# Kernel tuning notes

Measured on AMD Instinct MI355X. Metric: run time of the kernel, lower is better.

Reference implementation:

```python
import jax, jax.numpy as jnp
import numpy as np

HK, HV, D, K = 16, 32, 128, 4  # key heads, value heads, head dim, conv kernel
EPS = 1e-6


def setup_inputs() -> dict:
    key = jax.random.key(0)
    ks = jax.random.split(key, 8)
    B = 128
    C = D * (2 * HK + HV)  # qkv_size = 8192
    return {
        "mixed_qkv": jax.random.normal(ks[0], (B, C), jnp.float32),
        "a": jax.random.normal(ks[1], (B, HV), jnp.float32),
        "b": jax.random.normal(ks[2], (B, HV), jnp.float32),
        "conv_state": jax.random.normal(ks[3], (B, K - 1, C), jnp.float32),
        "ssm_state": jax.random.normal(ks[4], (B, HV, D, D), jnp.float32) * 0.1,
        "conv_weights": jax.random.normal(ks[5], (C, K), jnp.float32) * 0.1,
        "dt_bias": jax.random.normal(ks[6], (HV,), jnp.float32),
        "A_log": jax.random.normal(ks[7], (HV,), jnp.float32),
    }


def _l2norm(x):
    return x * jax.lax.rsqrt(jnp.sum(x * x, axis=-1, keepdims=True) + EPS)


def reference(mixed_qkv, a, b, conv_state, ssm_state, conv_weights, dt_bias, A_log):
    B = mixed_qkv.shape[0]
    # --- causal_conv1d_update (single decode token) ---
    # window: last K-1 cached tokens + current token, per channel
    window = jnp.concatenate([conv_state, mixed_qkv[:, None, :]], axis=1)  # [B, K, C]
    xconv = jax.nn.silu(jnp.einsum("bkc,ck->bc", window, conv_weights))  # [B, C]

    # --- split q/k/v heads ---
    qkv = xconv.reshape(B, 2 * HK + HV, D)
    q, k, v = qkv[:, :HK], qkv[:, HK:2 * HK], qkv[:, 2 * HK:]  # [B,HK,D]x2, [B,HV,D]

    # --- fused_gdn_gating ---
    g = -jnp.exp(A_log) * jax.nn.softplus(a + dt_bias)  # [B, HV]
    beta = jax.nn.sigmoid(b)                            # [B, HV]

    # --- fused_recurrent_gated_delta_rule, one step, qk l2norm + scale ---
    scale = D ** -0.5
    q = _l2norm(q) * scale
    k = _l2norm(k)
    rep = HV // HK  # GQA replication of q/k heads
    q = jnp.repeat(q, rep, axis=1)  # [B, HV, D]
    k = jnp.repeat(k, rep, axis=1)  # [B, HV, D]

    S = ssm_state * jnp.exp(g)[:, :, None, None]        # decay: [B,HV,Dv,Dk]
    kv_mem = jnp.einsum("bhvk,bhk->bhv", S, k)          # state readout along k
    delta = (v - kv_mem) * beta[:, :, None]             # delta rule correction
    S = S + delta[:, :, :, None] * k[:, :, None, :]     # rank-1 state update
    out = jnp.einsum("bhvk,bhk->bhv", S, q)             # [B, HV, Dv]
    return out
```

## Files before the change

kernel.cpp:

```cpp
#include <hip/hip_runtime.h>
#include <math.h>

#define HK 16
#define HV 32
#define DD 128
#define CC 8192
#define EPSN 1e-6f
#define QSCALE 0.08838834764831845f

__global__ __launch_bounds__(256) void prep_kernel(
    const float* __restrict__ mixed_qkv,
    const float* __restrict__ a_in,
    const float* __restrict__ b_in,
    const float* __restrict__ conv_state,
    const float* __restrict__ conv_weights,
    const float* __restrict__ dt_bias,
    const float* __restrict__ A_log,
    float* __restrict__ ws_q, float* __restrict__ ws_k, float* __restrict__ ws_v,
    float* __restrict__ ws_g, float* __restrict__ ws_beta)
{
    const int b   = blockIdx.x;
    const int tid = threadIdx.x;
    __shared__ float xconv[CC];

    const float* cs = conv_state + (size_t)b * 3 * CC;
    const float* mq = mixed_qkv  + (size_t)b * CC;

    for (int idx = tid; idx < CC; idx += 256) {
        float4 w = *reinterpret_cast<const float4*>(conv_weights + (size_t)idx * 4);
        float x = cs[idx] * w.x + cs[CC + idx] * w.y + cs[2 * CC + idx] * w.z
                + mq[idx] * w.w;
        xconv[idx] = x / (1.0f + expf(-x));
    }

    if (tid < HV) {
        float av = a_in[b * HV + tid] + dt_bias[tid];
        float sp = (av > 20.0f) ? av : log1pf(expf(av));
        ws_g[b * HV + tid]    = -expf(A_log[tid]) * sp;
        ws_beta[b * HV + tid] = 1.0f / (1.0f + expf(-b_in[b * HV + tid]));
    }
    __syncthreads();

    const int h   = tid >> 3;
    const int sub = tid & 7;
    const float* base = xconv + h * DD;
    float ssq = 0.f;
    #pragma unroll
    for (int i = 0; i < 16; ++i) {
        float xv = base[sub + 8 * i];
        ssq += xv * xv;
    }
    ssq += __shfl_xor(ssq, 1);
    ssq += __shfl_xor(ssq, 2);
    ssq += __shfl_xor(ssq, 4);
    float r = rsqrtf(ssq + EPSN);
    float factor = (h < HK) ? r * QSCALE : r;
    float* dst = (h < HK) ? (ws_q + ((size_t)b * HK + h) * DD)
                          : (ws_k + ((size_t)b * HK + (h - HK)) * DD);
    #pragma unroll
    for (int i = 0; i < 16; ++i)
        dst[sub + 8 * i] = base[sub + 8 * i] * factor;

    float* vdst = ws_v + (size_t)b * HV * DD;
    for (int idx = tid; idx < HV * DD; idx += 256)
        vdst[idx] = xconv[2 * HK * DD + idx];
}

__global__ __launch_bounds__(256) void update_kernel(
    const float* __restrict__ ssm_state,
    const float* __restrict__ ws_q, const float* __restrict__ ws_k,
    const float* __restrict__ ws_v, const float* __restrict__ ws_g,
    const float* __restrict__ ws_beta,
    float* __restrict__ out)
{
    const int bh  = blockIdx.x;
    const int b   = bh >> 5;
    const int h   = bh & 31;
    const int qh  = h >> 1;
    const int tid = threadIdx.x;
    const int col = (tid & 31) * 4;
    const int rb  = tid >> 5;

    __shared__ float dk[DD], dq[DD];

    const float4 kf = *reinterpret_cast<const float4*>(ws_k + ((size_t)b * HK + qh) * DD + col);
    const float4 qf = *reinterpret_cast<const float4*>(ws_q + ((size_t)b * HK + qh) * DD + col);

    float kq = kf.x * qf.x + kf.y * qf.y + kf.z * qf.z + kf.w * qf.w;
    kq += __shfl_xor(kq, 16);
    kq += __shfl_xor(kq, 8);
    kq += __shfl_xor(kq, 4);
    kq += __shfl_xor(kq, 2);
    kq += __shfl_xor(kq, 1);

    const float* S = ssm_state + (size_t)bh * DD * DD;
    #pragma unroll
    for (int c = 0; c < 16; ++c) {
        const int row = c * 8 + rb;
        float4 s = *reinterpret_cast<const float4*>(S + (size_t)row * DD + col);
        float pk = s.x * kf.x + s.y * kf.y + s.z * kf.z + s.w * kf.w;
        float pq = s.x * qf.x + s.y * qf.y + s.z * qf.z + s.w * qf.w;
        #pragma unroll
        for (int m = 16; m >= 1; m >>= 1) {
            pk += __shfl_xor(pk, m);
            pq += __shfl_xor(pq, m);
        }
        if ((tid & 31) == 0) { dk[row] = pk; dq[row] = pq; }
    }
    __syncthreads();

    if (tid < DD) {
        float eg   = expf(ws_g[bh]);
        float beta = ws_beta[bh];
        float vv   = ws_v[(size_t)bh * DD + tid];
        float delta = (vv - eg * dk[tid]) * beta;
        out[(size_t)bh * DD + tid] = eg * dq[tid] + delta * kq;
    }
}

extern "C" void kernel_launch(void* const* d_in, const int* in_sizes, int n_in,
                              void* d_out, int out_size, void* d_ws, size_t ws_size,
                              hipStream_t stream) {
    const float* mixed_qkv    = (const float*)d_in[0];
    const float* a_in         = (const float*)d_in[1];
    const float* b_in         = (const float*)d_in[2];
    const float* conv_state   = (const float*)d_in[3];
    const float* ssm_state    = (const float*)d_in[4];
    const float* conv_weights = (const float*)d_in[5];
    const float* dt_bias      = (const float*)d_in[6];
    const float* A_log        = (const float*)d_in[7];
    float* out = (float*)d_out;

    const int B = in_sizes[1] / HV;

    float* ws_q    = (float*)d_ws;
    float* ws_k    = ws_q + (size_t)B * HK * DD;
    float* ws_v    = ws_k + (size_t)B * HK * DD;
    float* ws_g    = ws_v + (size_t)B * HV * DD;
    float* ws_beta = ws_g + (size_t)B * HV;

    prep_kernel<<<B, 256, 0, stream>>>(mixed_qkv, a_in, b_in, conv_state,
                                       conv_weights, dt_bias, A_log,
                                       ws_q, ws_k, ws_v, ws_g, ws_beta);
    update_kernel<<<B * HV, 256, 0, stream>>>(ssm_state, ws_q, ws_k, ws_v,
                                              ws_g, ws_beta, out);
}
```

Before: 59.50 us.

## Fuse conv prep and state update into one kernel with a single matvec

```diff
diff --git a/kernel.cpp b/kernel.cpp
--- a/kernel.cpp
+++ b/kernel.cpp
@@ -1,121 +1,110 @@
 #include <hip/hip_runtime.h>
 #include <math.h>
 
-#define HK 16
-#define HV 32
-#define DD 128
-#define CC 8192
+#define HKn 16
+#define HVn 32
+#define DDn 128
+#define CCn 8192
 #define EPSN 1e-6f
 #define QSCALE 0.08838834764831845f
 
-__global__ __launch_bounds__(256) void prep_kernel(
+__global__ __launch_bounds__(256) void fused_gdn_decode(
     const float* __restrict__ mixed_qkv,
     const float* __restrict__ a_in,
     const float* __restrict__ b_in,
     const float* __restrict__ conv_state,
+    const float* __restrict__ ssm_state,
     const float* __restrict__ conv_weights,
     const float* __restrict__ dt_bias,
     const float* __restrict__ A_log,
-    float* __restrict__ ws_q, float* __restrict__ ws_k, float* __restrict__ ws_v,
-    float* __restrict__ ws_g, float* __restrict__ ws_beta)
+    float* __restrict__ out)
 {
-    const int b   = blockIdx.x;
-    const int tid = threadIdx.x;
-    __shared__ float xconv[CC];
+    const int bh = blockIdx.x;
+    const int b  = bh >> 5;
+    const int h  = bh & 31;
+    const int qh = h >> 1;
+    const int t  = threadIdx.x;
 
-    const float* cs = conv_state + (size_t)b * 3 * CC;
-    const float* mq = mixed_qkv  + (size_t)b * CC;
+    __shared__ float wv[DDn];
+    __shared__ float vb[DDn];
+    __shared__ float po[DDn];
+    __shared__ float red[6];
 
-    for (int idx = tid; idx < CC; idx += 256) {
-        float4 w = *reinterpret_cast<const float4*>(conv_weights + (size_t)idx * 4);
-        float x = cs[idx] * w.x + cs[CC + idx] * w.y + cs[2 * CC + idx] * w.z
-                + mq[idx] * w.w;
-        xconv[idx] = x / (1.0f + expf(-x));
-    }
+    const float* cs = conv_state + (size_t)b * 3 * CCn;
+    const float* mq = mixed_qkv  + (size_t)b * CCn;
 
-    if (tid < HV) {
-        float av = a_in[b * HV + tid] + dt_bias[tid];
-        float sp = (av > 20.0f) ? av : log1pf(expf(av));
-        ws_g[b * HV + tid]    = -expf(A_log[tid]) * sp;
-        ws_beta[b * HV + tid] = 1.0f / (1.0f + expf(-b_in[b * HV + tid]));
+    float xq = 0.f, xk = 0.f, bkq = 0.f;
+
+    if (t < DDn) {
+        const int cq = qh * DDn + t;
+        const int ck = (HKn + qh) * DDn + t;
+        float4 w = *reinterpret_cast<const float4*>(conv_weights + (size_t)cq * 4);
+        float x = cs[cq] * w.x + cs[CCn + cq] * w.y + cs[2 * CCn + cq] * w.z + mq[cq] * w.w;
+        xq = x / (1.f + expf(-x));
+        w = *reinterpret_cast<const float4*>(conv_weights + (size_t)ck * 4);
+        x = cs[ck] * w.x + cs[CCn + ck] * w.y + cs[2 * CCn + ck] * w.z + mq[ck] * w.w;
+        xk = x / (1.f + expf(-x));
+
+        float sqq = xq * xq, skk = xk * xk, sqk = xq * xk;
+        #pragma unroll
+        for (int m = 1; m <= 32; m <<= 1) {
+            sqq += __shfl_xor(sqq, m);
+            skk += __shfl_xor(skk, m);
+            sqk += __shfl_xor(sqk, m);
+        }
+        if ((t & 63) == 0) {
+            const int wv_ = t >> 6;
+            red[wv_ * 3 + 0] = sqq;
+            red[wv_ * 3 + 1] = skk;
+            red[wv_ * 3 + 2] = sqk;
+        }
+    } else {
+        const int cv = (2 * HKn + h) * DDn + (t - DDn);
+        float4 w = *reinterpret_cast<const float4*>(conv_weights + (size_t)cv * 4);
+        float x = cs[cv] * w.x + cs[CCn + cv] * w.y + cs[2 * CCn + cv] * w.z + mq[cv] * w.w;
+        vb[t - DDn] = x / (1.f + expf(-x));
     }
     __syncthreads();
 
-    const int h   = tid >> 3;
-    const int sub = tid & 7;
-    const float* base = xconv + h * DD;
-    float ssq = 0.f;
-    #pragma unroll
-    for (int i = 0; i < 16; ++i) {
-        float xv = base[sub + 8 * i];
-        ssq += xv * xv;
-    }
-    ssq += __shfl_xor(ssq, 1);
-    ssq += __shfl_xor(ssq, 2);
-    ssq += __shfl_xor(ssq, 4);
-    float r = rsqrtf(ssq + EPSN);
-    float factor = (h < HK) ? r * QSCALE : r;
-    float* dst = (h < HK) ? (ws_q + ((size_t)b * HK + h) * DD)
-                          : (ws_k + ((size_t)b * HK + (h - HK)) * DD);
-    #pragma unroll
-    for (int i = 0; i < 16; ++i)
-        dst[sub + 8 * i] = base[sub + 8 * i] * factor;
-
-    float* vdst = ws_v + (size_t)b * HV * DD;
-    for (int idx = tid; idx < HV * DD; idx += 256)
-        vdst[idx] = xconv[2 * HK * DD + idx];
-}
-
-__global__ __launch_bounds__(256) void update_kernel(
-    const float* __restrict__ ssm_state,
-    const float* __restrict__ ws_q, const float* __restrict__ ws_k,
-    const float* __restrict__ ws_v, const float* __restrict__ ws_g,
-    const float* __restrict__ ws_beta,
-    float* __restrict__ out)
-{
-    const int bh  = blockIdx.x;
-    const int b   = bh >> 5;
-    const int h   = bh & 31;
-    const int qh  = h >> 1;
-    const int tid = threadIdx.x;
-    const int col = (tid & 31) * 4;
-    const int rb  = tid >> 5;
-
-    __shared__ float dk[DD], dq[DD];
-
-    const float4 kf = *reinterpret_cast<const float4*>(ws_k + ((size_t)b * HK + qh) * DD + col);
-    const float4 qf = *reinterpret_cast<const float4*>(ws_q + ((size_t)b * HK + qh) * DD + col);
-
-    float kq = kf.x * qf.x + kf.y * qf.y + kf.z * qf.z + kf.w * qf.w;
-    kq += __shfl_xor(kq, 16);
-    kq += __shfl_xor(kq, 8);
-    kq += __shfl_xor(kq, 4);
-    kq += __shfl_xor(kq, 2);
-    kq += __shfl_xor(kq, 1);
-
-    const float* S = ssm_state + (size_t)bh * DD * DD;
-    #pragma unroll
-    for (int c = 0; c < 16; ++c) {
-        const int row = c * 8 + rb;
-        float4 s = *reinterpret_cast<const float4*>(S + (size_t)row * DD + col);
-        float pk = s.x * kf.x + s.y * kf.y + s.z * kf.z + s.w * kf.w;
-        float pq = s.x * qf.x + s.y * qf.y + s.z * qf.z + s.w * qf.w;
-        #pragma unroll
-        for (int m = 16; m >= 1; m >>= 1) {
-            pk += __shfl_xor(pk, m);
-            pq += __shfl_xor(pq, m);
-        }
-        if ((tid & 31) == 0) { dk[row] = pk; dq[row] = pq; }
+    if (t < DDn) {
+        const float sqq = red[0] + red[3];
+        const float skk = red[1] + red[4];
+        const float sqk = red[2] + red[5];
+        const float rq = rsqrtf(sqq + EPSN);
+        const float rk = rsqrtf(skk + EPSN);
+        const float kq = QSCALE * rq * rk * sqk;
+        const float av = a_in[b * HVn + h] + dt_bias[h];
+        const float sp = (av > 20.f) ? av : log1pf(expf(av));
+        const float eg = expf(-expf(A_log[h]) * sp);
+        const float beta = 1.f / (1.f + expf(-b_in[b * HVn + h]));
+        bkq = beta * kq;
+        wv[t] = eg * (rq * QSCALE * xq - bkq * rk * xk);
     }
     __syncthreads();
 
-    if (tid < DD) {
-        float eg   = expf(ws_g[bh]);
-        float beta = ws_beta[bh];
-        float vv   = ws_v[(size_t)bh * DD + tid];
-        float delta = (vv - eg * dk[tid]) * beta;
-        out[(size_t)bh * DD + tid] = eg * dq[tid] + delta * kq;
+    const int colg = t & 15;
+    const int rb   = t >> 4;
+    const float4 w0 = *reinterpret_cast<const float4*>(&wv[colg * 8]);
+    const float4 w1 = *reinterpret_cast<const float4*>(&wv[colg * 8 + 4]);
+    const float* S = ssm_state + (size_t)bh * DDn * DDn;
+    #pragma unroll
+    for (int c = 0; c < 8; ++c) {
+        const int row = c * 16 + rb;
+        const float* Sr = S + (size_t)row * DDn + colg * 8;
+        float4 s0 = *reinterpret_cast<const float4*>(Sr);
+        float4 s1 = *reinterpret_cast<const float4*>(Sr + 4);
+        float p = s0.x * w0.x + s0.y * w0.y + s0.z * w0.z + s0.w * w0.w
+                + s1.x * w1.x + s1.y * w1.y + s1.z * w1.z + s1.w * w1.w;
+        p += __shfl_xor(p, 8);
+        p += __shfl_xor(p, 4);
+        p += __shfl_xor(p, 2);
+        p += __shfl_xor(p, 1);
+        if (colg == 0) po[row] = p;
     }
+    __syncthreads();
+
+    if (t < DDn)
+        out[(size_t)bh * DDn + t] = po[t] + bkq * vb[t];
 }
 
 extern "C" void kernel_launch(void* const* d_in, const int* in_sizes, int n_in,
@@ -131,17 +120,9 @@
     const float* A_log        = (const float*)d_in[7];
     float* out = (float*)d_out;
 
-    const int B = in_sizes[1] / HV;
+    const int B = in_sizes[1] / HVn;
 
-    float* ws_q    = (float*)d_ws;
-    float* ws_k    = ws_q + (size_t)B * HK * DD;
-    float* ws_v    = ws_k + (size_t)B * HK * DD;
-    float* ws_g    = ws_v + (size_t)B * HV * DD;
-    float* ws_beta = ws_g + (size_t)B * HV;
-
-    prep_kernel<<<B, 256, 0, stream>>>(mixed_qkv, a_in, b_in, conv_state,
-                                       conv_weights, dt_bias, A_log,
-                                       ws_q, ws_k, ws_v, ws_g, ws_beta);
-    update_kernel<<<B * HV, 256, 0, stream>>>(ssm_state, ws_q, ws_k, ws_v,
-                                              ws_g, ws_beta, out);
+    fused_gdn_decode<<<B * HVn, 256, 0, stream>>>(
+        mixed_qkv, a_in, b_in, conv_state, ssm_state,
+        conv_weights, dt_bias, A_log, out);
 }
```

Measured after the change: 48.98 us. 17.7% less time.
